# Kernel tuning notes

Hardware: AMD Instinct MI355X
Metric: run time of the kernel (lower is better)

The kernel has to match this reference:

```python
import jax, jax.numpy as jnp
import numpy as np

B, C, H, W = 8, 128, 256, 256
WS = 8          # window_size (square)
HEADS = 4


def setup_inputs() -> dict:
    key = jax.random.key(0)
    k1, k2, k3, k4 = jax.random.split(key, 4)
    x = jax.random.normal(k1, (B, C, H, W), dtype=jnp.float32)
    # 1x1 convs are per-pixel matmuls; store weights as [out, in]
    w_qkv = jax.random.normal(k2, (3 * C, C), dtype=jnp.float32) * 0.05   # qkv conv, bias=False
    w_proj = jax.random.normal(k3, (C, C), dtype=jnp.float32) * 0.05      # proj conv weight
    b_proj = jax.random.normal(k4, (C,), dtype=jnp.float32) * 0.01        # proj conv bias
    return {"x": x, "w_qkv": w_qkv, "w_proj": w_proj, "b_proj": b_proj}


def reference(x, w_qkv, w_proj, b_proj):
    b, c, h, w = x.shape
    ws, heads = WS, HEADS
    d = c // heads
    scale = d ** -0.5
    hn, wn = h // ws, w // ws
    n = ws * ws  # tokens per window

    # unfold with kernel=stride=ws -> row-major window partition
    # [B,C,H,W] -> [B*hn*wn, C, n]
    xw = x.reshape(b, c, hn, ws, wn, ws)
    xw = xw.transpose(0, 2, 4, 1, 3, 5).reshape(b * hn * wn, c, n)

    # 1x1 conv QKV projection (no bias)
    qkv = jnp.einsum('oc,bcn->bon', w_qkv, xw)  # [Bw, 3C, n]
    q, k, v = jnp.split(qkv, 3, axis=1)
    q = q.reshape(-1, heads, d, n)
    k = k.reshape(-1, heads, d, n)
    v = v.reshape(-1, heads, d, n)

    # attn = (q^T k) * scale, softmax over keys
    attn = jax.nn.softmax(jnp.einsum('bhdn,bhdm->bhnm', q, k) * scale, axis=-1)
    out = jnp.einsum('bhnm,bhdm->bhdn', attn, v).reshape(-1, c, n)  # [Bw, C, n]

    # 1x1 proj conv with bias
    out = jnp.einsum('oc,bcn->bon', w_proj, out) + b_proj[None, :, None]

    # fold windows back: [Bw, C, n] -> [B, C, H, W]
    out = out.reshape(b, hn, wn, c, ws, ws)
    out = out.transpose(0, 3, 1, 4, 2, 5).reshape(b, c, h, w)
    return out
```

## Files before the change

### kernel.cpp

```cpp
#include <hip/hip_runtime.h>


#define HH    256
#define WWID  256
#define SCALE 0.17677669529663687f
#define LOG2E 1.44269504088896340736f

typedef float  f32x4  __attribute__((ext_vector_type(4)));
typedef __bf16 bf16x8 __attribute__((ext_vector_type(8)));
typedef __bf16 bf16x4 __attribute__((ext_vector_type(4)));
typedef __bf16 bf16x2 __attribute__((ext_vector_type(2)));
typedef short  s16x4  __attribute__((ext_vector_type(4)));

#define OT_BASE 16384

__device__ __forceinline__ s16x4 pack4(f32x4 v) {
  bf16x4 b = {(__bf16)v[0], (__bf16)v[1], (__bf16)v[2], (__bf16)v[3]};
  return __builtin_bit_cast(s16x4, b);
}

#if __has_builtin(__builtin_amdgcn_mfma_f32_16x16x16bf16_1k)
__device__ __forceinline__ f32x4 mfma16(s16x4 a, s16x4 b, f32x4 c) {
  return __builtin_amdgcn_mfma_f32_16x16x16bf16_1k(a, b, c, 0, 0, 0);
}
#else
__device__ __forceinline__ f32x4 mfma16(s16x4 a, s16x4 b, f32x4 c) {
  asm("v_mfma_f32_16x16x16_bf16 %0, %1, %2, %0" : "+v"(c) : "v"(a), "v"(b));
  return c;
}
#endif

__global__ void prep_weights(const float* __restrict__ wqkv,
                             const float* __restrict__ wproj,
                             __bf16* __restrict__ wbf) {
  int i = blockIdx.x * 256 + threadIdx.x;
  float v = (i < 49152) ? wqkv[i] : wproj[i - 49152];
  if (i < 16384) v *= SCALE * LOG2E;
  wbf[i] = (__bf16)v;
}

__global__ __launch_bounds__(256, 2)
void winattn_main(const float* __restrict__ x,
                  const __bf16* __restrict__ wqkv,
                  const __bf16* __restrict__ wproj,
                  const float* __restrict__ bproj,
                  float* __restrict__ out) {
  __shared__ __align__(16) char smem[32768];

  const int tid  = threadIdx.x;
  const int lane = tid & 63;
  const int wv   = tid >> 6;
  const int l15  = lane & 15;
  const int l4   = lane >> 4;

  const int bid = blockIdx.x;
  const int win = ((bid & 7) << 10) | (bid >> 3);
  const int b   = win >> 10;
  const int wy  = (win >> 5) & 31;
  const int wx  = win & 31;
  const int gy0 = wy * 8, gx0 = wx * 8;

  #pragma unroll
  for (int it = 0; it < 4; ++it) {
    int idx   = tid + it * 256;
    int cpair = idx >> 4;
    int r     = idx & 15;
    int ty    = r >> 1, tx4 = r & 1;
    const float* px = x + (((size_t)(b * 128 + 2 * cpair) * HH + gy0 + ty) * WWID + gx0 + tx4 * 4);
    float4 v0 = *(const float4*)px;
    float4 v1 = *(const float4*)(px + (size_t)HH * WWID);
    float a0[4] = {v0.x, v0.y, v0.z, v0.w};
    float a1[4] = {v1.x, v1.y, v1.z, v1.w};
    #pragma unroll
    for (int i = 0; i < 4; ++i) {
      int tok = ty * 8 + tx4 * 4 + i;
      bf16x2 w2 = {(__bf16)a0[i], (__bf16)a1[i]};
      int byte = (tok * 256 + cpair * 4) ^ ((tok & 15) << 4);
      *(bf16x2*)(smem + byte) = w2;
    }
  }
  __syncthreads();

  #define XT_AFRAG(mt, kt) \
    (*(const bf16x8*)(smem + ((((mt) * 16 + l15) * 256 + ((kt) * 32 + l4 * 8) * 2) ^ \
                              ((((mt) * 16 + l15) & 15) << 4))))
  #define OT_AFRAG(mt, kt) \
    (*(const bf16x8*)(smem + OT_BASE + ((((mt) * 16 + l15) * 256 + ((kt) * 32 + l4 * 8) * 2) ^ \
                              ((((mt) * 16 + l15) & 15) << 4))))

  s16x4 qb[2][4];
  {
    f32x4 acc[2][4] = {};
    #pragma unroll
    for (int kt = 0; kt < 4; ++kt) {
      bf16x8 xf[4];
      #pragma unroll
      for (int mt = 0; mt < 4; ++mt) xf[mt] = XT_AFRAG(mt, kt);
      #pragma unroll
      for (int nt2 = 0; nt2 < 2; ++nt2) {
        bf16x8 w = *(const bf16x8*)(wqkv + (size_t)(wv * 32 + nt2 * 16 + l15) * 128 + kt * 32 + l4 * 8);
        #pragma unroll
        for (int mt = 0; mt < 4; ++mt)
          acc[nt2][mt] = __builtin_amdgcn_mfma_f32_16x16x32_bf16(w, xf[mt], acc[nt2][mt], 0, 0, 0);
      }
    }
    #pragma unroll
    for (int nt2 = 0; nt2 < 2; ++nt2)
      #pragma unroll
      for (int mt = 0; mt < 4; ++mt) qb[nt2][mt] = pack4(acc[nt2][mt]);
  }

  s16x4 kb[2][4];
  {
    f32x4 acc[2][4] = {};
    #pragma unroll
    for (int kt = 0; kt < 4; ++kt) {
      bf16x8 xf[4];
      #pragma unroll
      for (int mt = 0; mt < 4; ++mt) xf[mt] = XT_AFRAG(mt, kt);
      #pragma unroll
      for (int nt2 = 0; nt2 < 2; ++nt2) {
        bf16x8 w = *(const bf16x8*)(wqkv + (size_t)(128 + wv * 32 + nt2 * 16 + l15) * 128 + kt * 32 + l4 * 8);
        #pragma unroll
        for (int mt = 0; mt < 4; ++mt)
          acc[nt2][mt] = __builtin_amdgcn_mfma_f32_16x16x32_bf16(w, xf[mt], acc[nt2][mt], 0, 0, 0);
      }
    }
    #pragma unroll
    for (int nt2 = 0; nt2 < 2; ++nt2)
      #pragma unroll
      for (int mt = 0; mt < 4; ++mt) kb[nt2][mt] = pack4(acc[nt2][mt]);
  }

  s16x4 ap[4][4];
  #pragma unroll
  for (int t = 0; t < 4; ++t) {
    f32x4 st[4];
    #pragma unroll
    for (int m = 0; m < 4; ++m) {
      f32x4 z = {0.f, 0.f, 0.f, 0.f};
      st[m] = mfma16(kb[0][m], qb[0][t], z);
      st[m] = mfma16(kb[1][m], qb[1][t], st[m]);
    }
    float mx = st[0][0];
    #pragma unroll
    for (int m = 0; m < 4; ++m)
      #pragma unroll
      for (int r = 0; r < 4; ++r) mx = fmaxf(mx, st[m][r]);
    mx = fmaxf(mx, __shfl_xor(mx, 16));
    mx = fmaxf(mx, __shfl_xor(mx, 32));
    float p[4][4];
    float sm = 0.f;
    #pragma unroll
    for (int m = 0; m < 4; ++m)
      #pragma unroll
      for (int r = 0; r < 4; ++r) {
        p[m][r] = __builtin_amdgcn_exp2f(st[m][r] - mx);
        sm += p[m][r];
      }
    sm += __shfl_xor(sm, 16);
    sm += __shfl_xor(sm, 32);
    float inv = __builtin_amdgcn_rcpf(sm);
    #pragma unroll
    for (int m = 0; m < 4; ++m) {
      f32x4 pn = {p[m][0] * inv, p[m][1] * inv, p[m][2] * inv, p[m][3] * inv};
      ap[t][m] = pack4(pn);
    }
  }

  s16x4 vb[2][4];
  {
    f32x4 acc[2][4] = {};
    #pragma unroll
    for (int kt = 0; kt < 4; ++kt) {
      bf16x8 xf[4];
      #pragma unroll
      for (int mt = 0; mt < 4; ++mt) xf[mt] = XT_AFRAG(mt, kt);
      #pragma unroll
      for (int nt2 = 0; nt2 < 2; ++nt2) {
        bf16x8 w = *(const bf16x8*)(wqkv + (size_t)(256 + wv * 32 + nt2 * 16 + l15) * 128 + kt * 32 + l4 * 8);
        #pragma unroll
        for (int mt = 0; mt < 4; ++mt)
          acc[nt2][mt] = __builtin_amdgcn_mfma_f32_16x16x32_bf16(xf[mt], w, acc[nt2][mt], 0, 0, 0);
      }
    }
    #pragma unroll
    for (int nt2 = 0; nt2 < 2; ++nt2)
      #pragma unroll
      for (int mt = 0; mt < 4; ++mt) vb[nt2][mt] = pack4(acc[nt2][mt]);
  }

  #pragma unroll
  for (int t = 0; t < 4; ++t) {
    f32x4 o0 = {0.f, 0.f, 0.f, 0.f}, o1 = {0.f, 0.f, 0.f, 0.f};
    #pragma unroll
    for (int m = 0; m < 4; ++m) {
      o0 = mfma16(ap[t][m], vb[0][m], o0);
      o1 = mfma16(ap[t][m], vb[1][m], o1);
    }
    #pragma unroll
    for (int r = 0; r < 4; ++r) {
      int tok = t * 16 + l4 * 4 + r;
      int c0  = wv * 32 + l15;
      int sw  = (tok & 15) << 4;
      *(__bf16*)(smem + OT_BASE + ((tok * 256 + c0 * 2) ^ sw))         = (__bf16)o0[r];
      *(__bf16*)(smem + OT_BASE + ((tok * 256 + (c0 + 16) * 2) ^ sw))  = (__bf16)o1[r];
    }
  }
  __syncthreads();

  f32x4 pacc[2][4] = {};
  #pragma unroll
  for (int kt = 0; kt < 4; ++kt) {
    bf16x8 of[4];
    #pragma unroll
    for (int mt = 0; mt < 4; ++mt) of[mt] = OT_AFRAG(mt, kt);
    #pragma unroll
    for (int i = 0; i < 2; ++i) {
      bf16x8 wp = *(const bf16x8*)(wproj + (size_t)((wv * 2 + i) * 16 + l15) * 128 + kt * 32 + l4 * 8);
      #pragma unroll
      for (int mt = 0; mt < 4; ++mt)
        pacc[i][mt] = __builtin_amdgcn_mfma_f32_16x16x32_bf16(of[mt], wp, pacc[i][mt], 0, 0, 0);
    }
  }

  #pragma unroll
  for (int i = 0; i < 2; ++i) {
    int o = (wv * 2 + i) * 16 + l15;
    float bias = bproj[o];
    float* obase = out + (size_t)(b * 128 + o) * ((size_t)HH * WWID) + gy0 * WWID + gx0;
    #pragma unroll
    for (int mt = 0; mt < 4; ++mt) {
      int tok0 = mt * 16 + l4 * 4;
      int ty = tok0 >> 3, tx0 = tok0 & 7;
      float4 f = {pacc[i][mt][0] + bias, pacc[i][mt][1] + bias,
                  pacc[i][mt][2] + bias, pacc[i][mt][3] + bias};
      *(float4*)(obase + ty * WWID + tx0) = f;
    }
  }
}

extern "C" void kernel_launch(void* const* d_in, const int* in_sizes, int n_in,
                              void* d_out, int out_size, void* d_ws, size_t ws_size,
                              hipStream_t stream) {
  const float* x     = (const float*)d_in[0];
  const float* wqkv  = (const float*)d_in[1];
  const float* wproj = (const float*)d_in[2];
  const float* bproj = (const float*)d_in[3];
  float* out = (float*)d_out;

  __bf16* wbf = (__bf16*)d_ws;
  prep_weights<<<256, 256, 0, stream>>>(wqkv, wproj, wbf);
  winattn_main<<<8192, 256, 0, stream>>>(x, wbf, wbf + 49152, bproj, out);
}
```

Measured before the change: 271.6 us.

## Split each head across two waves with K/V shared via LDS

Blocks grow from 4 to 8 waves. Each pair of waves handles one head, and each wave computes Q/K/V for half of the 64 tokens. K and V tiles go to swizzled LDS and each wave reads back the full K/V after a barrier. The attention output reuses the input-staging LDS region, and each wave computes 16 output channels of the projection. This shortens the per-wave serial MFMA chain and lowers register pressure. In exchange it adds LDS traffic, an extra barrier and 48KB of LDS per block, which may limit occupancy.

Result: slower. 328.8 us (+21.1%).

```diff
diff --git a/kernel.cpp b/kernel.cpp
--- a/kernel.cpp
+++ b/kernel.cpp
@@ -12,7 +12,8 @@
 typedef __bf16 bf16x2 __attribute__((ext_vector_type(2)));
 typedef short  s16x4  __attribute__((ext_vector_type(4)));
 
-#define OT_BASE 16384
+#define K_BASE 16384
+#define V_BASE 32768
 
 __device__ __forceinline__ s16x4 pack4(f32x4 v) {
   bf16x4 b = {(__bf16)v[0], (__bf16)v[1], (__bf16)v[2], (__bf16)v[3]};
@@ -39,17 +40,19 @@
   wbf[i] = (__bf16)v;
 }
 
-__global__ __launch_bounds__(256, 2)
+__global__ __launch_bounds__(512, 4)
 void winattn_main(const float* __restrict__ x,
                   const __bf16* __restrict__ wqkv,
                   const __bf16* __restrict__ wproj,
                   const float* __restrict__ bproj,
                   float* __restrict__ out) {
-  __shared__ __align__(16) char smem[32768];
+  __shared__ __align__(16) char smem[49152];
 
   const int tid  = threadIdx.x;
   const int lane = tid & 63;
   const int wv   = tid >> 6;
+  const int h    = wv >> 1;
+  const int s    = wv & 1;
   const int l15  = lane & 15;
   const int l4   = lane >> 4;
 
@@ -61,8 +64,8 @@
   const int gy0 = wy * 8, gx0 = wx * 8;
 
   #pragma unroll
-  for (int it = 0; it < 4; ++it) {
-    int idx   = tid + it * 256;
+  for (int it = 0; it < 2; ++it) {
+    int idx   = tid + it * 512;
     int cpair = idx >> 4;
     int r     = idx & 15;
     int ty    = r >> 1, tx4 = r & 1;
@@ -84,57 +87,95 @@
   #define XT_AFRAG(mt, kt) \
     (*(const bf16x8*)(smem + ((((mt) * 16 + l15) * 256 + ((kt) * 32 + l4 * 8) * 2) ^ \
                               ((((mt) * 16 + l15) & 15) << 4))))
-  #define OT_AFRAG(mt, kt) \
-    (*(const bf16x8*)(smem + OT_BASE + ((((mt) * 16 + l15) * 256 + ((kt) * 32 + l4 * 8) * 2) ^ \
-                              ((((mt) * 16 + l15) & 15) << 4))))
-
-  s16x4 qb[2][4];
-  {
-    f32x4 acc[2][4] = {};
+
+  s16x4 qb[2][2];
+  {
+    f32x4 acc[2][2] = {};
     #pragma unroll
     for (int kt = 0; kt < 4; ++kt) {
-      bf16x8 xf[4];
-      #pragma unroll
-      for (int mt = 0; mt < 4; ++mt) xf[mt] = XT_AFRAG(mt, kt);
+      bf16x8 xf[2];
+      #pragma unroll
+      for (int mq = 0; mq < 2; ++mq) xf[mq] = XT_AFRAG(s * 2 + mq, kt);
       #pragma unroll
       for (int nt2 = 0; nt2 < 2; ++nt2) {
-        bf16x8 w = *(const bf16x8*)(wqkv + (size_t)(wv * 32 + nt2 * 16 + l15) * 128 + kt * 32 + l4 * 8);
+        bf16x8 w = *(const bf16x8*)(wqkv + (size_t)(h * 32 + nt2 * 16 + l15) * 128 + kt * 32 + l4 * 8);
         #pragma unroll
-        for (int mt = 0; mt < 4; ++mt)
-          acc[nt2][mt] = __builtin_amdgcn_mfma_f32_16x16x32_bf16(w, xf[mt], acc[nt2][mt], 0, 0, 0);
+        for (int mq = 0; mq < 2; ++mq)
+          acc[nt2][mq] = __builtin_amdgcn_mfma_f32_16x16x32_bf16(w, xf[mq], acc[nt2][mq], 0, 0, 0);
       }
     }
     #pragma unroll
     for (int nt2 = 0; nt2 < 2; ++nt2)
       #pragma unroll
-      for (int mt = 0; mt < 4; ++mt) qb[nt2][mt] = pack4(acc[nt2][mt]);
-  }
-
-  s16x4 kb[2][4];
-  {
-    f32x4 acc[2][4] = {};
+      for (int mq = 0; mq < 2; ++mq) qb[nt2][mq] = pack4(acc[nt2][mq]);
+  }
+
+  {
+    f32x4 acc[2][2] = {};
     #pragma unroll
     for (int kt = 0; kt < 4; ++kt) {
-      bf16x8 xf[4];
-      #pragma unroll
-      for (int mt = 0; mt < 4; ++mt) xf[mt] = XT_AFRAG(mt, kt);
+      bf16x8 xf[2];
+      #pragma unroll
+      for (int mk = 0; mk < 2; ++mk) xf[mk] = XT_AFRAG(s * 2 + mk, kt);
       #pragma unroll
       for (int nt2 = 0; nt2 < 2; ++nt2) {
-        bf16x8 w = *(const bf16x8*)(wqkv + (size_t)(128 + wv * 32 + nt2 * 16 + l15) * 128 + kt * 32 + l4 * 8);
+        bf16x8 w = *(const bf16x8*)(wqkv + (size_t)(128 + h * 32 + nt2 * 16 + l15) * 128 + kt * 32 + l4 * 8);
         #pragma unroll
-        for (int mt = 0; mt < 4; ++mt)
-          acc[nt2][mt] = __builtin_amdgcn_mfma_f32_16x16x32_bf16(w, xf[mt], acc[nt2][mt], 0, 0, 0);
+        for (int mk = 0; mk < 2; ++mk)
+          acc[nt2][mk] = __builtin_amdgcn_mfma_f32_16x16x32_bf16(w, xf[mk], acc[nt2][mk], 0, 0, 0);
       }
     }
     #pragma unroll
     for (int nt2 = 0; nt2 < 2; ++nt2)
       #pragma unroll
-      for (int mt = 0; mt < 4; ++mt) kb[nt2][mt] = pack4(acc[nt2][mt]);
-  }
-
-  s16x4 ap[4][4];
-  #pragma unroll
-  for (int t = 0; t < 4; ++t) {
+      for (int mk = 0; mk < 2; ++mk) {
+        int tok = (s * 2 + mk) * 16 + l15;
+        int d0  = nt2 * 16 + l4 * 4;
+        int byte = K_BASE + h * 4096 + ((tok * 64 + d0 * 2) ^ ((tok & 3) << 4));
+        *(s16x4*)(smem + byte) = pack4(acc[nt2][mk]);
+      }
+  }
+
+  {
+    f32x4 acc[2][2] = {};
+    #pragma unroll
+    for (int kt = 0; kt < 4; ++kt) {
+      bf16x8 xf[2];
+      #pragma unroll
+      for (int mv = 0; mv < 2; ++mv) xf[mv] = XT_AFRAG(s * 2 + mv, kt);
+      #pragma unroll
+      for (int nt2 = 0; nt2 < 2; ++nt2) {
+        bf16x8 w = *(const bf16x8*)(wqkv + (size_t)(256 + h * 32 + nt2 * 16 + l15) * 128 + kt * 32 + l4 * 8);
+        #pragma unroll
+        for (int mv = 0; mv < 2; ++mv)
+          acc[nt2][mv] = __builtin_amdgcn_mfma_f32_16x16x32_bf16(xf[mv], w, acc[nt2][mv], 0, 0, 0);
+      }
+    }
+    #pragma unroll
+    for (int nt2 = 0; nt2 < 2; ++nt2)
+      #pragma unroll
+      for (int mv = 0; mv < 2; ++mv) {
+        int d    = nt2 * 16 + l15;
+        int tok0 = (s * 2 + mv) * 16 + l4 * 4;
+        int byte = V_BASE + h * 4096 + ((d * 128 + tok0 * 2) ^ ((d & 7) << 4));
+        *(s16x4*)(smem + byte) = pack4(acc[nt2][mv]);
+      }
+  }
+  __syncthreads();
+
+  s16x4 kb[2][4], vb[2][4];
+  #pragma unroll
+  for (int nt2 = 0; nt2 < 2; ++nt2)
+    #pragma unroll
+    for (int m = 0; m < 4; ++m) {
+      int tok = m * 16 + l15, d0 = nt2 * 16 + l4 * 4;
+      kb[nt2][m] = *(const s16x4*)(smem + K_BASE + h * 4096 + ((tok * 64 + d0 * 2) ^ ((tok & 3) << 4)));
+      int d = nt2 * 16 + l15, tok0 = m * 16 + l4 * 4;
+      vb[nt2][m] = *(const s16x4*)(smem + V_BASE + h * 4096 + ((d * 128 + tok0 * 2) ^ ((d & 7) << 4)));
+    }
+
+  #pragma unroll
+  for (int t = 0; t < 2; ++t) {
     f32x4 st[4];
     #pragma unroll
     for (int m = 0; m < 4; ++m) {
@@ -161,80 +202,51 @@
     sm += __shfl_xor(sm, 16);
     sm += __shfl_xor(sm, 32);
     float inv = __builtin_amdgcn_rcpf(sm);
+    s16x4 ap[4];
     #pragma unroll
     for (int m = 0; m < 4; ++m) {
       f32x4 pn = {p[m][0] * inv, p[m][1] * inv, p[m][2] * inv, p[m][3] * inv};
-      ap[t][m] = pack4(pn);
-    }
-  }
-
-  s16x4 vb[2][4];
-  {
-    f32x4 acc[2][4] = {};
-    #pragma unroll
-    for (int kt = 0; kt < 4; ++kt) {
-      bf16x8 xf[4];
-      #pragma unroll
-      for (int mt = 0; mt < 4; ++mt) xf[mt] = XT_AFRAG(mt, kt);
-      #pragma unroll
-      for (int nt2 = 0; nt2 < 2; ++nt2) {
-        bf16x8 w = *(const bf16x8*)(wqkv + (size_t)(256 + wv * 32 + nt2 * 16 + l15) * 128 + kt * 32 + l4 * 8);
-        #pragma unroll
-        for (int mt = 0; mt < 4; ++mt)
-          acc[nt2][mt] = __builtin_amdgcn_mfma_f32_16x16x32_bf16(xf[mt], w, acc[nt2][mt], 0, 0, 0);
-      }
-    }
-    #pragma unroll
-    for (int nt2 = 0; nt2 < 2; ++nt2)
-      #pragma unroll
-      for (int mt = 0; mt < 4; ++mt) vb[nt2][mt] = pack4(acc[nt2][mt]);
-  }
-
-  #pragma unroll
-  for (int t = 0; t < 4; ++t) {
+      ap[m] = pack4(pn);
+    }
     f32x4 o0 = {0.f, 0.f, 0.f, 0.f}, o1 = {0.f, 0.f, 0.f, 0.f};
     #pragma unroll
     for (int m = 0; m < 4; ++m) {
-      o0 = mfma16(ap[t][m], vb[0][m], o0);
-      o1 = mfma16(ap[t][m], vb[1][m], o1);
+      o0 = mfma16(ap[m], vb[0][m], o0);
+      o1 = mfma16(ap[m], vb[1][m], o1);
     }
     #pragma unroll
     for (int r = 0; r < 4; ++r) {
-      int tok = t * 16 + l4 * 4 + r;
-      int c0  = wv * 32 + l15;
+      int tok = s * 32 + t * 16 + l4 * 4 + r;
+      int c0  = h * 32 + l15;
       int sw  = (tok & 15) << 4;
-      *(__bf16*)(smem + OT_BASE + ((tok * 256 + c0 * 2) ^ sw))         = (__bf16)o0[r];
-      *(__bf16*)(smem + OT_BASE + ((tok * 256 + (c0 + 16) * 2) ^ sw))  = (__bf16)o1[r];
+      *(__bf16*)(smem + ((tok * 256 + c0 * 2) ^ sw))        = (__bf16)o0[r];
+      *(__bf16*)(smem + ((tok * 256 + (c0 + 16) * 2) ^ sw)) = (__bf16)o1[r];
     }
   }
   __syncthreads();
 
-  f32x4 pacc[2][4] = {};
+  f32x4 pacc[4] = {};
   #pragma unroll
   for (int kt = 0; kt < 4; ++kt) {
     bf16x8 of[4];
     #pragma unroll
-    for (int mt = 0; mt < 4; ++mt) of[mt] = OT_AFRAG(mt, kt);
-    #pragma unroll
-    for (int i = 0; i < 2; ++i) {
-      bf16x8 wp = *(const bf16x8*)(wproj + (size_t)((wv * 2 + i) * 16 + l15) * 128 + kt * 32 + l4 * 8);
-      #pragma unroll
-      for (int mt = 0; mt < 4; ++mt)
-        pacc[i][mt] = __builtin_amdgcn_mfma_f32_16x16x32_bf16(of[mt], wp, pacc[i][mt], 0, 0, 0);
-    }
-  }
-
-  #pragma unroll
-  for (int i = 0; i < 2; ++i) {
-    int o = (wv * 2 + i) * 16 + l15;
+    for (int mt = 0; mt < 4; ++mt) of[mt] = XT_AFRAG(mt, kt);
+    bf16x8 wp = *(const bf16x8*)(wproj + (size_t)(wv * 16 + l15) * 128 + kt * 32 + l4 * 8);
+    #pragma unroll
+    for (int mt = 0; mt < 4; ++mt)
+      pacc[mt] = __builtin_amdgcn_mfma_f32_16x16x32_bf16(of[mt], wp, pacc[mt], 0, 0, 0);
+  }
+
+  {
+    int o = wv * 16 + l15;
     float bias = bproj[o];
     float* obase = out + (size_t)(b * 128 + o) * ((size_t)HH * WWID) + gy0 * WWID + gx0;
     #pragma unroll
     for (int mt = 0; mt < 4; ++mt) {
       int tok0 = mt * 16 + l4 * 4;
       int ty = tok0 >> 3, tx0 = tok0 & 7;
-      float4 f = {pacc[i][mt][0] + bias, pacc[i][mt][1] + bias,
-                  pacc[i][mt][2] + bias, pacc[i][mt][3] + bias};
+      float4 f = {pacc[mt][0] + bias, pacc[mt][1] + bias,
+                  pacc[mt][2] + bias, pacc[mt][3] + bias};
       *(float4*)(obase + ty * WWID + tx0) = f;
     }
   }
@@ -251,5 +263,5 @@
 
   __bf16* wbf = (__bf16*)d_ws;
   prep_weights<<<256, 256, 0, stream>>>(wqkv, wproj, wbf);
-  winattn_main<<<8192, 256, 0, stream>>>(x, wbf, wbf + 49152, bproj, out);
-}
+  winattn_main<<<8192, 512, 0, stream>>>(x, wbf, wbf + 49152, bproj, out);
+}
```
